# Performance work log

Measured on AMD Instinct MI355X. Metric: run time of the kernel, lower is better.

## Reference

```python
import jax, jax.numpy as jnp
import numpy as np


def _windowed_attn(q, k, v, window_size, num_heads):
    # q, k, v: [B, T, D] with T % window_size == 0
    B, T, D = q.shape
    hd = D // num_heads
    scale = 1.0 / np.sqrt(hd).astype(np.float32)
    nw = T // window_size
    # [B, nw, w, H, hd]
    qh = q.reshape(B, nw, window_size, num_heads, hd)
    kh = k.reshape(B, nw, window_size, num_heads, hd)
    vh = v.reshape(B, nw, window_size, num_heads, hd)
    # attention scores per window: [B, nw, H, w, w]
    attn = jnp.einsum('bnqhd,bnkhd->bnhqk', qh, kh) * scale
    attn = jax.nn.softmax(attn, axis=-1)
    out = jnp.einsum('bnhqk,bnkhd->bnqhd', attn, vh)
    return out.reshape(B, T, D)


def setup_inputs() -> dict:
    key = jax.random.key(0)
    ks = jax.random.split(key, 6)
    B, D = 8, 512
    T1, T2 = 4096, 2048
    return {
        'q1': jax.random.normal(ks[0], (B, T1, D), dtype=jnp.float32),
        'k1': jax.random.normal(ks[1], (B, T1, D), dtype=jnp.float32),
        'v1': jax.random.normal(ks[2], (B, T1, D), dtype=jnp.float32),
        'q2': jax.random.normal(ks[3], (B, T2, D), dtype=jnp.float32),
        'k2': jax.random.normal(ks[4], (B, T2, D), dtype=jnp.float32),
        'v2': jax.random.normal(ks[5], (B, T2, D), dtype=jnp.float32),
        'window_size': 128,
        'num_heads': 8,
    }


def reference(q1, k1, v1, q2, k2, v2, window_size, num_heads):
    out1 = _windowed_attn(q1, k1, v1, window_size, num_heads)
    out2 = _windowed_attn(q2, k2, v2, window_size, num_heads)
    return (out1, out2)
```

## Files before the change

### kernel.cpp

```cpp
#include <hip/hip_runtime.h>
#include <hip/hip_bf16.h>

typedef __attribute__((ext_vector_type(4))) float f32x4;
typedef __attribute__((ext_vector_type(16))) float f32x16;
typedef __attribute__((ext_vector_type(8))) short bf16x8;

#define NH 8
#define HD 64
#define WSZ 128
#define DM 512

__device__ __forceinline__ unsigned int pk2bf(float lo, float hi) {
    union { __hip_bfloat162 h; unsigned int u; } r;
    r.h = __float22bfloat162_rn(make_float2(lo, hi));
    return r.u;
}

__device__ __forceinline__ bf16x8 pack8(f32x4 a, f32x4 b) {
    union { unsigned int u[4]; bf16x8 v; } r;
    r.u[0] = pk2bf(a[0], a[1]);
    r.u[1] = pk2bf(a[2], a[3]);
    r.u[2] = pk2bf(b[0], b[1]);
    r.u[3] = pk2bf(b[2], b[3]);
    return r.v;
}

__global__ __launch_bounds__(256, 4) void wattn_kernel(
    const float* __restrict__ q1, const float* __restrict__ k1,
    const float* __restrict__ v1, float* __restrict__ o1, int nw1,
    const float* __restrict__ q2, const float* __restrict__ k2,
    const float* __restrict__ v2, float* __restrict__ o2, int nw2,
    int nblk1, int cpx)
{
    __shared__ __align__(16) unsigned short Kl[128 * 64];
    __shared__ __align__(16) unsigned short Vt[64 * 128];

    const int t = threadIdx.x;
    const int lane = t & 63;
    const int wid = t >> 6;
    const int hi = lane >> 5;
    const int c = lane & 31;

    int bid = (blockIdx.x & 7) * cpx + (blockIdx.x >> 3);

    const float *q, *k, *v; float* o; int nw;
    if (bid < nblk1) { q = q1; k = k1; v = v1; o = o1; nw = nw1; }
    else { bid -= nblk1; q = q2; k = k2; v = v2; o = o2; nw = nw2; }

    const int h = bid & (NH - 1);
    const int w = (bid / NH) % nw;
    const int b = (bid / NH) / nw;

    const size_t row0 = ((size_t)b * nw + w) * WSZ;
    const float* Qp = q + row0 * DM + h * HD;
    const float* Kp = k + row0 * DM + h * HD;
    const float* Vp = v + row0 * DM + h * HD;
    float* Op = o + row0 * DM + h * HD;

#pragma unroll
    for (int i = 0; i < 4; ++i) {
        int row = i * 32 + (t >> 3);
        int colf = (t & 7) * 8;
        const float* src = Kp + (size_t)row * DM + colf;
        f32x4 a = *reinterpret_cast<const f32x4*>(src);
        f32x4 bq = *reinterpret_cast<const f32x4*>(src + 4);
        int base = row * 64, sw = (row & 7) << 3;
        *reinterpret_cast<unsigned int*>(&Kl[base + (colf ^ sw)]) = pk2bf(a[0], a[1]);
        *reinterpret_cast<unsigned int*>(&Kl[base + ((colf + 2) ^ sw)]) = pk2bf(a[2], a[3]);
        *reinterpret_cast<unsigned int*>(&Kl[base + ((colf + 4) ^ sw)]) = pk2bf(bq[0], bq[1]);
        *reinterpret_cast<unsigned int*>(&Kl[base + ((colf + 6) ^ sw)]) = pk2bf(bq[2], bq[3]);
    }

#pragma unroll
    for (int i = 0; i < 4; ++i) {
        int rp = i * 16 + (t >> 4);
        int dc = (t & 15) * 4;
        f32x4 va = *reinterpret_cast<const f32x4*>(Vp + (size_t)(2 * rp) * DM + dc);
        f32x4 vb = *reinterpret_cast<const f32x4*>(Vp + (size_t)(2 * rp + 1) * DM + dc);
#pragma unroll
        for (int j = 0; j < 4; ++j) {
            int d = dc + j;
            int idx = d * 128 + ((2 * rp) ^ (((d >> 1) & 7) << 3));
            *reinterpret_cast<unsigned int*>(&Vt[idx]) = pk2bf(va[j], vb[j]);
        }
    }

    const int qbase = wid * 32;
    bf16x8 qf[4];
#pragma unroll
    for (int ks = 0; ks < 4; ++ks) {
        const float* src = Qp + (size_t)(qbase + c) * DM + ks * 16 + hi * 8;
        f32x4 a = *reinterpret_cast<const f32x4*>(src);
        f32x4 bq = *reinterpret_cast<const f32x4*>(src + 4);
        qf[ks] = pack8(a, bq);
    }

    __syncthreads();

    f32x16 acc[4] = {};
#pragma unroll
    for (int ks = 0; ks < 4; ++ks) {
#pragma unroll
        for (int mf = 0; mf < 4; ++mf) {
            const bf16x8 kf = *reinterpret_cast<const bf16x8*>(
                &Kl[(mf * 32 + c) * 64 + ((ks * 16 + hi * 8) ^ ((c & 7) << 3))]);
            acc[mf] = __builtin_amdgcn_mfma_f32_32x32x16_bf16(kf, qf[ks], acc[mf], 0, 0, 0);
        }
    }

    const float CEXP = 0.125f * 1.4426950408889634f;
    float mxa = fmaxf(acc[0][0], acc[1][0]);
    float mxb = fmaxf(acc[2][0], acc[3][0]);
#pragma unroll
    for (int e = 1; e < 16; ++e) {
        mxa = fmaxf(mxa, fmaxf(acc[0][e], acc[1][e]));
        mxb = fmaxf(mxb, fmaxf(acc[2][e], acc[3][e]));
    }
    float mx = fmaxf(mxa, mxb);
    mx = fmaxf(mx, __shfl_xor(mx, 32));
    const float mxc = mx * CEXP;
    float s0 = 0.f, s1 = 0.f, s2 = 0.f, s3 = 0.f;
#pragma unroll
    for (int e = 0; e < 16; ++e) {
        float p0 = exp2f(acc[0][e] * CEXP - mxc);
        float p1 = exp2f(acc[1][e] * CEXP - mxc);
        float p2 = exp2f(acc[2][e] * CEXP - mxc);
        float p3 = exp2f(acc[3][e] * CEXP - mxc);
        acc[0][e] = p0; acc[1][e] = p1; acc[2][e] = p2; acc[3][e] = p3;
        s0 += p0; s1 += p1; s2 += p2; s3 += p3;
    }
    float sum = (s0 + s1) + (s2 + s3);
    sum += __shfl_xor(sum, 32);
    const float rinv = 1.0f / sum;

    f32x16 oacc[2] = {};
#pragma unroll
    for (int f = 0; f < 4; ++f) {
#pragma unroll
        for (int p = 0; p < 2; ++p) {
            const int kb = f * 2 + p;
            unsigned int U0 = pk2bf(acc[f][8 * p + 0], acc[f][8 * p + 1]);
            unsigned int U1 = pk2bf(acc[f][8 * p + 2], acc[f][8 * p + 3]);
            unsigned int U2 = pk2bf(acc[f][8 * p + 4], acc[f][8 * p + 5]);
            unsigned int U3 = pk2bf(acc[f][8 * p + 6], acc[f][8 * p + 7]);
            asm volatile("v_permlane32_swap_b32 %0, %1" : "+v"(U0), "+v"(U2));
            asm volatile("v_permlane32_swap_b32 %0, %1" : "+v"(U1), "+v"(U3));
            union { unsigned int u[4]; bf16x8 v; } A;
            A.u[0] = U0; A.u[1] = U1; A.u[2] = U2; A.u[3] = U3;
#pragma unroll
            for (int nf = 0; nf < 2; ++nf) {
                const int d = nf * 32 + c;
                const bf16x8 vf = *reinterpret_cast<const bf16x8*>(
                    &Vt[d * 128 + ((kb * 16 + hi * 8) ^ (((d >> 1) & 7) << 3))]);
                oacc[nf] = __builtin_amdgcn_mfma_f32_32x32x16_bf16(A.v, vf, oacc[nf], 0, 0, 0);
            }
        }
    }

#pragma unroll
    for (int reg = 0; reg < 16; ++reg) {
        const int qr = (reg & 3) + 8 * (reg >> 2) + 4 * hi;
        const float rv = __shfl(rinv, qr);
#pragma unroll
        for (int nf = 0; nf < 2; ++nf) {
            Op[(size_t)(qbase + qr) * DM + nf * 32 + c] = oacc[nf][reg] * rv;
        }
    }
}

extern "C" void kernel_launch(void* const* d_in, const int* in_sizes, int n_in,
                              void* d_out, int out_size, void* d_ws, size_t ws_size,
                              hipStream_t stream) {
    const float* q1 = (const float*)d_in[0];
    const float* k1 = (const float*)d_in[1];
    const float* v1 = (const float*)d_in[2];
    const float* q2 = (const float*)d_in[3];
    const float* k2 = (const float*)d_in[4];
    const float* v2 = (const float*)d_in[5];

    const int B = 8;
    const int nw1 = in_sizes[0] / (B * DM * WSZ);
    const int nw2 = in_sizes[3] / (B * DM * WSZ);

    float* o1 = (float*)d_out;
    float* o2 = o1 + (size_t)in_sizes[0];

    const int nblk1 = B * nw1 * NH;
    const int nblk2 = B * nw2 * NH;
    const int ntot = nblk1 + nblk2;
    const int cpx = ntot / 8;

    wattn_kernel<<<dim3(ntot), dim3(256), 0, stream>>>(
        q1, k1, v1, o1, nw1, q2, k2, v2, o2, nw2, nblk1, cpx);
}
```

Baseline: 90.54 us.

## Stage K and V as fp32 in LDS via direct global-to-LDS loads

Result: faster. 88.51 us (-2.2%).

```diff
diff --git a/kernel.cpp b/kernel.cpp
--- a/kernel.cpp
+++ b/kernel.cpp
@@ -9,6 +9,9 @@
 #define HD 64
 #define WSZ 128
 #define DM 512
+
+typedef __attribute__((address_space(3))) void lds_t;
+typedef const __attribute__((address_space(1))) void gbl_t;
 
 __device__ __forceinline__ unsigned int pk2bf(float lo, float hi) {
     union { __hip_bfloat162 h; unsigned int u; } r;
@@ -25,15 +28,15 @@
     return r.v;
 }
 
-__global__ __launch_bounds__(256, 4) void wattn_kernel(
+__global__ __launch_bounds__(256, 2) void wattn_kernel(
     const float* __restrict__ q1, const float* __restrict__ k1,
     const float* __restrict__ v1, float* __restrict__ o1, int nw1,
     const float* __restrict__ q2, const float* __restrict__ k2,
     const float* __restrict__ v2, float* __restrict__ o2, int nw2,
-    int nblk1, int cpx)
+    int nblk1)
 {
-    __shared__ __align__(16) unsigned short Kl[128 * 64];
-    __shared__ __align__(16) unsigned short Vt[64 * 128];
+    __shared__ __align__(16) float Kl[128 * 64];
+    __shared__ __align__(16) float Vl[128 * 64];
 
     const int t = threadIdx.x;
     const int lane = t & 63;
@@ -41,8 +44,7 @@
     const int hi = lane >> 5;
     const int c = lane & 31;
 
-    int bid = (blockIdx.x & 7) * cpx + (blockIdx.x >> 3);
-
+    int bid = blockIdx.x;
     const float *q, *k, *v; float* o; int nw;
     if (bid < nblk1) { q = q1; k = k1; v = v1; o = o1; nw = nw1; }
     else { bid -= nblk1; q = q2; k = k2; v = v2; o = o2; nw = nw2; }
@@ -57,35 +59,21 @@
     const float* Vp = v + row0 * DM + h * HD;
     float* Op = o + row0 * DM + h * HD;
 
+    const int qbase = wid * 32;
+
 #pragma unroll
-    for (int i = 0; i < 4; ++i) {
-        int row = i * 32 + (t >> 3);
-        int colf = (t & 7) * 8;
-        const float* src = Kp + (size_t)row * DM + colf;
-        f32x4 a = *reinterpret_cast<const f32x4*>(src);
-        f32x4 bq = *reinterpret_cast<const f32x4*>(src + 4);
-        int base = row * 64, sw = (row & 7) << 3;
-        *reinterpret_cast<unsigned int*>(&Kl[base + (colf ^ sw)]) = pk2bf(a[0], a[1]);
-        *reinterpret_cast<unsigned int*>(&Kl[base + ((colf + 2) ^ sw)]) = pk2bf(a[2], a[3]);
-        *reinterpret_cast<unsigned int*>(&Kl[base + ((colf + 4) ^ sw)]) = pk2bf(bq[0], bq[1]);
-        *reinterpret_cast<unsigned int*>(&Kl[base + ((colf + 6) ^ sw)]) = pk2bf(bq[2], bq[3]);
+    for (int ii = 0; ii < 8; ++ii) {
+        const int idx = wid * 8 + ii;
+        const int row = idx * 4 + (lane >> 4);
+        const int gs = lane & 15;
+        const float* gk = Kp + (size_t)row * DM + ((gs ^ (row & 15)) << 2);
+        const float* gv = Vp + (size_t)row * DM + (gs << 2);
+        __builtin_amdgcn_global_load_lds((gbl_t*)gk,
+            (lds_t*)((char*)Kl + idx * 1024), 16, 0, 0);
+        __builtin_amdgcn_global_load_lds((gbl_t*)gv,
+            (lds_t*)((char*)Vl + idx * 1024), 16, 0, 0);
     }
 
-#pragma unroll
-    for (int i = 0; i < 4; ++i) {
-        int rp = i * 16 + (t >> 4);
-        int dc = (t & 15) * 4;
-        f32x4 va = *reinterpret_cast<const f32x4*>(Vp + (size_t)(2 * rp) * DM + dc);
-        f32x4 vb = *reinterpret_cast<const f32x4*>(Vp + (size_t)(2 * rp + 1) * DM + dc);
-#pragma unroll
-        for (int j = 0; j < 4; ++j) {
-            int d = dc + j;
-            int idx = d * 128 + ((2 * rp) ^ (((d >> 1) & 7) << 3));
-            *reinterpret_cast<unsigned int*>(&Vt[idx]) = pk2bf(va[j], vb[j]);
-        }
-    }
-
-    const int qbase = wid * 32;
     bf16x8 qf[4];
 #pragma unroll
     for (int ks = 0; ks < 4; ++ks) {
@@ -102,8 +90,12 @@
     for (int ks = 0; ks < 4; ++ks) {
 #pragma unroll
         for (int mf = 0; mf < 4; ++mf) {
-            const bf16x8 kf = *reinterpret_cast<const bf16x8*>(
-                &Kl[(mf * 32 + c) * 64 + ((ks * 16 + hi * 8) ^ ((c & 7) << 3))]);
+            const int row = mf * 32 + c;
+            const int r15 = c & 15;
+            const int g0 = ks * 4 + hi * 2;
+            f32x4 a = *reinterpret_cast<const f32x4*>(&Kl[row * 64 + ((g0 ^ r15) << 2)]);
+            f32x4 bq = *reinterpret_cast<const f32x4*>(&Kl[row * 64 + (((g0 + 1) ^ r15) << 2)]);
+            const bf16x8 kf = pack8(a, bq);
             acc[mf] = __builtin_amdgcn_mfma_f32_32x32x16_bf16(kf, qf[ks], acc[mf], 0, 0, 0);
         }
     }
@@ -138,7 +130,7 @@
     for (int f = 0; f < 4; ++f) {
 #pragma unroll
         for (int p = 0; p < 2; ++p) {
-            const int kb = f * 2 + p;
+            const int kb2 = f * 2 + p;
             unsigned int U0 = pk2bf(acc[f][8 * p + 0], acc[f][8 * p + 1]);
             unsigned int U1 = pk2bf(acc[f][8 * p + 2], acc[f][8 * p + 3]);
             unsigned int U2 = pk2bf(acc[f][8 * p + 4], acc[f][8 * p + 5]);
@@ -147,12 +139,16 @@
             asm volatile("v_permlane32_swap_b32 %0, %1" : "+v"(U1), "+v"(U3));
             union { unsigned int u[4]; bf16x8 v; } A;
             A.u[0] = U0; A.u[1] = U1; A.u[2] = U2; A.u[3] = U3;
+            const int k0 = kb2 * 16 + hi * 8;
 #pragma unroll
             for (int nf = 0; nf < 2; ++nf) {
-                const int d = nf * 32 + c;
-                const bf16x8 vf = *reinterpret_cast<const bf16x8*>(
-                    &Vt[d * 128 + ((kb * 16 + hi * 8) ^ (((d >> 1) & 7) << 3))]);
-                oacc[nf] = __builtin_amdgcn_mfma_f32_32x32x16_bf16(A.v, vf, oacc[nf], 0, 0, 0);
+                const float* vb = &Vl[k0 * 64 + nf * 32 + c];
+                union { unsigned int u[4]; bf16x8 v; } V8;
+                V8.u[0] = pk2bf(vb[0 * 64], vb[1 * 64]);
+                V8.u[1] = pk2bf(vb[2 * 64], vb[3 * 64]);
+                V8.u[2] = pk2bf(vb[4 * 64], vb[5 * 64]);
+                V8.u[3] = pk2bf(vb[6 * 64], vb[7 * 64]);
+                oacc[nf] = __builtin_amdgcn_mfma_f32_32x32x16_bf16(A.v, V8.v, oacc[nf], 0, 0, 0);
             }
         }
     }
@@ -187,9 +183,7 @@
 
     const int nblk1 = B * nw1 * NH;
     const int nblk2 = B * nw2 * NH;
-    const int ntot = nblk1 + nblk2;
-    const int cpx = ntot / 8;
 
-    wattn_kernel<<<dim3(ntot), dim3(256), 0, stream>>>(
-        q1, k1, v1, o1, nw1, q2, k2, v2, o2, nw2, nblk1, cpx);
+    wattn_kernel<<<dim3(nblk1 + nblk2), dim3(256), 0, stream>>>(
+        q1, k1, v1, o1, nw1, q2, k2, v2, o2, nw2, nblk1);
 }
```
